# Kernel tuning notes

Hardware: AMD Instinct MI355X
Metric: run time of the kernel (lower is better)

## Reference

```python
import jax, jax.numpy as jnp
import numpy as np

NUM_CLASSES = 81
NMS_THRESHOLD = 0.4
MAX_BOXES = 300
NEG = -1e9  # score used to mark suppressed / background boxes


def setup_inputs() -> dict:
    key = jax.random.key(0)
    k1, k2, k3, k4, k5 = jax.random.split(key, 5)
    N = 300000
    # realistic boxes: centers in [0,800), sizes in [1,101)
    cx = jax.random.uniform(k1, (N,), jnp.float32) * 800.0
    cy = jax.random.uniform(k2, (N,), jnp.float32) * 800.0
    w = jax.random.uniform(k3, (N,), jnp.float32) * 100.0 + 1.0
    h = jax.random.uniform(k4, (N,), jnp.float32) * 100.0 + 1.0
    boxes = jnp.stack([cx - w / 2, cy - h / 2, cx + w / 2, cy + h / 2], axis=-1)
    boxes = boxes[None]  # [1, N, 4]
    classification = jax.random.normal(k5, (1, N, NUM_CLASSES), jnp.float32)
    return {"boxes": boxes, "classification": classification}


def _nms_select(boxes, scores, max_boxes, iou_threshold):
    # boxes: [N,4] (x1,y1,x2,y2); scores: [N]. Greedy NMS, fixed max_boxes iterations.
    x1, y1, x2, y2 = boxes[:, 0], boxes[:, 1], boxes[:, 2], boxes[:, 3]
    areas = jnp.maximum(x2 - x1, 0.0) * jnp.maximum(y2 - y1, 0.0)

    def body(scores_c, _):
        idx = jnp.argmax(scores_c)
        valid = scores_c[idx] > NEG / 2
        b = boxes[idx]
        xx1 = jnp.maximum(b[0], x1)
        yy1 = jnp.maximum(b[1], y1)
        xx2 = jnp.minimum(b[2], x2)
        yy2 = jnp.minimum(b[3], y2)
        inter = jnp.maximum(xx2 - xx1, 0.0) * jnp.maximum(yy2 - yy1, 0.0)
        union = areas[idx] + areas - inter
        iou = inter / jnp.maximum(union, 1e-8)
        # suppress everything overlapping the selected box (includes itself, iou=1)
        new_scores = jnp.where(iou > iou_threshold, NEG, scores_c)
        return new_scores, (idx, valid)

    _, (idxs, valids) = jax.lax.scan(body, scores, None, length=max_boxes)
    return idxs, valids


def reference(boxes, classification):
    b = boxes.reshape(-1, 4)                      # [N,4]
    cls = classification.reshape(-1, NUM_CLASSES)  # [N,C]
    scores = jnp.max(cls, axis=1)                  # [N]
    labels = jnp.argmax(cls, axis=1)               # [N]
    # filter background (label==0) by masking scores instead of dynamic gather
    scores = jnp.where(labels > 0, scores, NEG)
    idxs, valid = _nms_select(b, scores, MAX_BOXES, NMS_THRESHOLD)
    v = valid[:, None].astype(b.dtype)
    out_boxes = b[idxs] * v                        # [max_boxes,4], zero-padded
    out_cls = cls[idxs] * v                        # [max_boxes,C], zero-padded
    return out_boxes[None], out_cls[None]
```

## Files before the change

kernel.cpp:

```cpp
#include <hip/hip_runtime.h>
#include <stdint.h>

#define NUM_CLASSES 81
#define MAX_BOXES 300
#define NEG_SCORE (-1000000000.0f)
#define IOU_THR 0.4f
#define MMAX 2048
#define MWORDS (MMAX / 64)

static constexpr size_t OFF_SCORES = 0;
static constexpr size_t OFF_CAREA  = 0x1F0000;
static constexpr size_t OFF_COARSE = 0x200000;
static constexpr size_t OFF_FINE   = 0x201000;
static constexpr size_t OFF_CTRL   = 0x202000;
static constexpr size_t OFF_RANK   = 0x203000;
static constexpr size_t OFF_KEYS   = 0x208000;
static constexpr size_t OFF_CIDX   = 0x210000;
static constexpr size_t OFF_CBOX   = 0x214000;
static constexpr size_t OFF_ACC    = 0x224000;
static constexpr size_t OFF_MATRIX = 0x228000;

__device__ __forceinline__ uint32_t float_ordered(float f) {
    uint32_t b = __float_as_uint(f);
    return (b & 0x80000000u) ? ~b : (b | 0x80000000u);
}

__device__ __forceinline__ uint64_t readlane_u64(uint64_t v, int srclane) {
    uint32_t lo = (uint32_t)__builtin_amdgcn_readlane((int)(uint32_t)v, srclane);
    uint32_t hi = (uint32_t)__builtin_amdgcn_readlane((int)(uint32_t)(v >> 32), srclane);
    return ((uint64_t)hi << 32) | lo;
}

__global__ void score_kernel(const float* __restrict__ cls, float* __restrict__ scores,
                             uint32_t* __restrict__ coarse, uint32_t* __restrict__ fine,
                             uint32_t* __restrict__ ctrl, uint32_t* __restrict__ rank, int n) {
    if (blockIdx.x == 0) {
        int t = threadIdx.x;
        if (t < 256) { coarse[t] = 0; fine[t] = 0; }
        if (t < 8) ctrl[t] = 0;
        for (int r = t; r < MMAX; r += 256) rank[r] = 0;
    }
    const int q = threadIdx.x & 15;
    const int box = blockIdx.x * 16 + (threadIdx.x >> 4);
    const int cbox = box < n ? box : n - 1;
    const float* row = cls + (size_t)cbox * NUM_CLASSES;

    float v[5];
    #pragma unroll
    for (int it = 0; it < 5; ++it) v[it] = row[it * 16 + q];
    float e80 = row[80];

    float m = v[0];
    #pragma unroll
    for (int it = 1; it < 5; ++it) m = fmaxf(m, v[it]);
    m = (q == 15) ? fmaxf(m, e80) : m;
    m = fmaxf(m, __shfl_xor(m, 1));
    m = fmaxf(m, __shfl_xor(m, 2));
    m = fmaxf(m, __shfl_xor(m, 4));
    m = fmaxf(m, __shfl_xor(m, 8));

    if (q == 0 && box < n) {
        scores[box] = (v[0] == m) ? NEG_SCORE : m;
    }
}

__global__ void coarse_hist_kernel(const float* __restrict__ scores, uint32_t* __restrict__ coarse, int n) {
    __shared__ uint32_t h[256];
    for (int t = threadIdx.x; t < 256; t += blockDim.x) h[t] = 0;
    __syncthreads();
    for (int i = blockIdx.x * blockDim.x + threadIdx.x; i < n; i += gridDim.x * blockDim.x) {
        uint32_t o = float_ordered(scores[i]);
        atomicAdd(&h[o >> 24], 1u);
    }
    __syncthreads();
    for (int t = threadIdx.x; t < 256; t += blockDim.x)
        if (h[t]) atomicAdd(&coarse[t], h[t]);
}

__device__ __forceinline__ int select_coarse(const uint32_t* coarse, uint32_t* above_out) {
    uint32_t s = 0;
    for (int c = 255; c >= 0; --c) {
        uint32_t sc = s + coarse[c];
        if (sc > MMAX) { *above_out = s; return c; }
        s = sc;
    }
    *above_out = s;
    return -1;
}

__global__ void fine_hist_kernel(const float* __restrict__ scores, const uint32_t* __restrict__ coarse,
                                 uint32_t* __restrict__ fine, int n) {
    __shared__ int sC;
    __shared__ uint32_t h[256];
    if (threadIdx.x == 0) {
        uint32_t above;
        sC = select_coarse(coarse, &above);
    }
    for (int t = threadIdx.x; t < 256; t += blockDim.x) h[t] = 0;
    __syncthreads();
    int C = sC;
    if (C < 0) return;
    for (int i = blockIdx.x * blockDim.x + threadIdx.x; i < n; i += gridDim.x * blockDim.x) {
        uint32_t o = float_ordered(scores[i]);
        if ((int)(o >> 24) == C) atomicAdd(&h[(o >> 16) & 255u], 1u);
    }
    __syncthreads();
    for (int t = threadIdx.x; t < 256; t += blockDim.x)
        if (h[t]) atomicAdd(&fine[t], h[t]);
}

__global__ void compact_kernel(const float* __restrict__ scores, const uint32_t* __restrict__ coarse,
                               const uint32_t* __restrict__ fine, uint32_t* __restrict__ ctrl,
                               uint64_t* __restrict__ keys, int n) {
    __shared__ uint32_t sThr;
    if (threadIdx.x == 0) {
        uint32_t above;
        int C = select_coarse(coarse, &above);
        uint32_t thr;
        if (C < 0) {
            thr = 0;
        } else {
            uint32_t R = MMAX - above;
            uint32_t g = 0, F = 0;
            for (int f = 255; f >= 0; --f) {
                uint32_t gf = g + fine[f];
                if (gf > R) { F = (uint32_t)f + 1u; break; }
                g = gf;
            }
            thr = ((uint32_t)C << 8) | F;
        }
        sThr = thr;
    }
    __syncthreads();
    uint32_t thr = sThr;
    for (int i = blockIdx.x * blockDim.x + threadIdx.x; i < n; i += gridDim.x * blockDim.x) {
        uint32_t o = float_ordered(scores[i]);
        if ((o >> 16) >= thr) {
            uint32_t pos = atomicAdd(&ctrl[0], 1u);
            if (pos < MMAX)
                keys[pos] = ((uint64_t)o << 32) | (uint32_t)(~(uint32_t)i);
        }
    }
}

__global__ void rank_partial_kernel(const uint64_t* __restrict__ keys, const uint32_t* __restrict__ ctrl,
                                    uint32_t* __restrict__ rank) {
    __shared__ uint64_t kk[256];
    int M = (int)ctrl[0]; if (M > MMAX) M = MMAX;
    int cbase = blockIdx.x * 256;
    int jbase = blockIdx.y * 256;
    if (cbase >= M || jbase >= M) return;
    int t = threadIdx.x;
    int j = jbase + t;
    kk[t] = (j < M) ? keys[j] : 0ull;
    __syncthreads();
    int c = cbase + t;
    if (c >= M) return;
    uint64_t k = keys[c];
    int cnt = 0;
    #pragma unroll 8
    for (int u = 0; u < 256; ++u) cnt += (kk[u] > k) ? 1 : 0;
    if (cnt) atomicAdd(&rank[c], (uint32_t)cnt);
}

__global__ void scatter_kernel(const uint64_t* __restrict__ keys, const uint32_t* __restrict__ rank,
                               const uint32_t* __restrict__ ctrl, const float* __restrict__ boxes,
                               int* __restrict__ csorted_idx, float4* __restrict__ csorted_box,
                               float* __restrict__ careas) {
    int M = (int)ctrl[0]; if (M > MMAX) M = MMAX;
    int c = blockIdx.x * blockDim.x + threadIdx.x;
    if (c >= M) return;
    uint64_t k = keys[c];
    uint32_t r = rank[c];
    uint32_t idx = ~(uint32_t)k;
    float4 b = *(const float4*)(boxes + (size_t)idx * 4);
    csorted_idx[r] = (int)idx;
    csorted_box[r] = b;
    careas[r] = fmaxf(b.z - b.x, 0.f) * fmaxf(b.w - b.y, 0.f);
}

__global__ void matrix_kernel(const float4* __restrict__ cbox, const float* __restrict__ careas,
                              const uint32_t* __restrict__ ctrl, uint64_t* __restrict__ matrix) {
    int i = blockIdx.x;
    int M = (int)ctrl[0]; if (M > MMAX) M = MMAX;
    if (i >= M) return;
    int lane = threadIdx.x & 63;
    int wave = threadIdx.x >> 6;
    float4 bi = cbox[i];
    float ai = careas[i];
    int w0 = i >> 6;
    for (int w = w0 + wave; w < MWORDS; w += 4) {
        int j = (w << 6) | lane;
        bool sup = false;
        if (j < M) {
            float4 bj = cbox[j];
            float xx1 = fmaxf(bi.x, bj.x);
            float yy1 = fmaxf(bi.y, bj.y);
            float xx2 = fminf(bi.z, bj.z);
            float yy2 = fminf(bi.w, bj.w);
            float inter = fmaxf(xx2 - xx1, 0.f) * fmaxf(yy2 - yy1, 0.f);
            float uni = ai + careas[j] - inter;
            float iou = inter / fmaxf(uni, 1e-8f);
            sup = iou > IOU_THR;
        }
        uint64_t word = __ballot(sup ? 1 : 0);
        if (lane == 0) matrix[(size_t)i * MWORDS + w] = word;
    }
}

typedef const uint32_t __attribute__((address_space(1)))* glb_u32p;
typedef uint32_t __attribute__((address_space(3)))* lds_u32p;

__global__ void __launch_bounds__(64) scan_kernel(
    const uint64_t* __restrict__ matrix, uint32_t* __restrict__ ctrl,
    int* __restrict__ accepted) {
    __shared__ uint64_t sbuf[2][64][MWORDS];
    const int lane = threadIdx.x;
    const int l31 = lane & 31;
    int M = (int)ctrl[0]; if (M > MMAX) M = MMAX;
    uint64_t removed = 0;
    uint64_t wrd = 0;
    int acc = 0;

#define STAGE(BI, BASE)                                                            \
    {                                                                              \
        _Pragma("unroll")                                                          \
        for (int r_ = 0; r_ < 64; ++r_) {                                          \
            const uint32_t* gsrc =                                                 \
                (const uint32_t*)(matrix + (size_t)((BASE) + r_) * MWORDS) + lane; \
            __builtin_amdgcn_global_load_lds((glb_u32p)gsrc,                       \
                                             (lds_u32p)&sbuf[BI][r_][0], 4, 0, 0); \
        }                                                                          \
    }

#define PROCESS(BI, BASE)                                                          \
    {                                                                              \
        uint64_t W[16];                                                            \
        _Pragma("unroll")                                                          \
        for (int w_ = 0; w_ < 16; ++w_) W[w_] = sbuf[BI][w_][l31];                 \
        _Pragma("unroll")                                                          \
        for (int r_ = 0; r_ < 64; ++r_) {                                          \
            int i_ = (BASE) + r_;                                                  \
            uint64_t row = W[r_ & 15];                                             \
            if (r_ + 16 < 64) W[r_ & 15] = sbuf[BI][r_ + 16][l31];                 \
            if (r_ == 0) wrd = readlane_u64(removed, i_ >> 6);                     \
            if (i_ < M && acc < MAX_BOXES && !((wrd >> (i_ & 63)) & 1ull)) {       \
                if (lane == 0) accepted[acc] = i_;                                 \
                removed |= row;                                                    \
                wrd = readlane_u64(removed, i_ >> 6);                              \
                ++acc;                                                             \
            }                                                                      \
        }                                                                          \
    }

    int nblocks = (M + 63) >> 6;
    if (nblocks > 0) {
        STAGE(0, 0);
        asm volatile("s_waitcnt vmcnt(0)" ::: "memory");
        int bi = 0;
        for (int b = 0; b < nblocks && acc < MAX_BOXES; ++b) {
            if (b + 1 < nblocks) STAGE(bi ^ 1, (b + 1) << 6);
            PROCESS(bi, b << 6);
            asm volatile("s_waitcnt vmcnt(0)" ::: "memory");
            bi ^= 1;
        }
    }
#undef STAGE
#undef PROCESS
    if (lane == 0) ctrl[1] = (uint32_t)acc;
}

__global__ void output_kernel(const float* __restrict__ boxes, const float* __restrict__ cls,
                              const int* __restrict__ csorted_idx, const int* __restrict__ accepted,
                              const uint32_t* __restrict__ ctrl, float* __restrict__ out, int total) {
    int e = blockIdx.x * blockDim.x + threadIdx.x;
    if (e >= total) return;
    int acc = (int)ctrl[1];
    float val = 0.0f;
    if (e < MAX_BOXES * 4) {
        int s = e >> 2, f = e & 3;
        if (s < acc) {
            int orig = csorted_idx[accepted[s]];
            val = boxes[(size_t)orig * 4 + f];
        }
    } else {
        int e2 = e - MAX_BOXES * 4;
        int s = e2 / NUM_CLASSES;
        int c = e2 - s * NUM_CLASSES;
        if (s < acc) {
            int orig = csorted_idx[accepted[s]];
            val = cls[(size_t)orig * NUM_CLASSES + c];
        }
    }
    out[e] = val;
}

extern "C" void kernel_launch(void* const* d_in, const int* in_sizes, int n_in,
                              void* d_out, int out_size, void* d_ws, size_t ws_size,
                              hipStream_t stream) {
    const float* boxes = (const float*)d_in[0];
    const float* cls   = (const float*)d_in[1];
    float* out = (float*)d_out;
    const int N = in_sizes[0] / 4;

    char* ws = (char*)d_ws;
    float*     scores      = (float*)(ws + OFF_SCORES);
    float*     careas      = (float*)(ws + OFF_CAREA);
    uint32_t*  coarse      = (uint32_t*)(ws + OFF_COARSE);
    uint32_t*  fine        = (uint32_t*)(ws + OFF_FINE);
    uint32_t*  ctrl        = (uint32_t*)(ws + OFF_CTRL);
    uint32_t*  rank        = (uint32_t*)(ws + OFF_RANK);
    uint64_t*  keys        = (uint64_t*)(ws + OFF_KEYS);
    int*       csorted_idx = (int*)(ws + OFF_CIDX);
    float4*    csorted_box = (float4*)(ws + OFF_CBOX);
    int*       accepted    = (int*)(ws + OFF_ACC);
    uint64_t*  matrix      = (uint64_t*)(ws + OFF_MATRIX);

    score_kernel<<<(N + 15) / 16, 256, 0, stream>>>(cls, scores, coarse, fine, ctrl, rank, N);
    coarse_hist_kernel<<<256, 256, 0, stream>>>(scores, coarse, N);
    fine_hist_kernel<<<256, 256, 0, stream>>>(scores, coarse, fine, N);
    compact_kernel<<<512, 256, 0, stream>>>(scores, coarse, fine, ctrl, keys, N);
    rank_partial_kernel<<<dim3(MMAX / 256, MMAX / 256), 256, 0, stream>>>(keys, ctrl, rank);
    scatter_kernel<<<MMAX / 256, 256, 0, stream>>>(keys, rank, ctrl, boxes, csorted_idx,
                                                   csorted_box, careas);
    matrix_kernel<<<MMAX, 256, 0, stream>>>(csorted_box, careas, ctrl, matrix);
    scan_kernel<<<1, 64, 0, stream>>>(matrix, ctrl, accepted);
    output_kernel<<<(out_size + 255) / 256, 256, 0, stream>>>(boxes, cls, csorted_idx, accepted,
                                                              ctrl, out, out_size);
}
```

Measured before the change: 108.6 us.

## Fuse IoU matrix, greedy scan and output gather into one last-block kernel

Merges the suppression-matrix, sequential scan and output kernels into a single launch. Each block computes its matrix row, then an agent-scope atomic counter elects the last finished block, which runs the greedy scan with accepted indices kept in LDS and writes the output itself. This removes two kernel launches and the global round-trip for accepted indices. In exchange the output gather runs in one block instead of a full grid, and correctness depends on the counter in ctrl[4] being reset each call.

Result: slower. 220.1 us (+102.7%).

```diff
diff --git a/kernel.cpp b/kernel.cpp
--- a/kernel.cpp
+++ b/kernel.cpp
@@ -17,7 +17,6 @@
 static constexpr size_t OFF_KEYS   = 0x208000;
 static constexpr size_t OFF_CIDX   = 0x210000;
 static constexpr size_t OFF_CBOX   = 0x214000;
-static constexpr size_t OFF_ACC    = 0x224000;
 static constexpr size_t OFF_MATRIX = 0x228000;
 
 __device__ __forceinline__ uint32_t float_ordered(float f) {
@@ -179,48 +178,62 @@
     careas[r] = fmaxf(b.z - b.x, 0.f) * fmaxf(b.w - b.y, 0.f);
 }
 
-__global__ void matrix_kernel(const float4* __restrict__ cbox, const float* __restrict__ careas,
-                              const uint32_t* __restrict__ ctrl, uint64_t* __restrict__ matrix) {
-    int i = blockIdx.x;
-    int M = (int)ctrl[0]; if (M > MMAX) M = MMAX;
-    if (i >= M) return;
-    int lane = threadIdx.x & 63;
-    int wave = threadIdx.x >> 6;
-    float4 bi = cbox[i];
-    float ai = careas[i];
-    int w0 = i >> 6;
-    for (int w = w0 + wave; w < MWORDS; w += 4) {
-        int j = (w << 6) | lane;
-        bool sup = false;
-        if (j < M) {
-            float4 bj = cbox[j];
-            float xx1 = fmaxf(bi.x, bj.x);
-            float yy1 = fmaxf(bi.y, bj.y);
-            float xx2 = fminf(bi.z, bj.z);
-            float yy2 = fminf(bi.w, bj.w);
-            float inter = fmaxf(xx2 - xx1, 0.f) * fmaxf(yy2 - yy1, 0.f);
-            float uni = ai + careas[j] - inter;
-            float iou = inter / fmaxf(uni, 1e-8f);
-            sup = iou > IOU_THR;
-        }
-        uint64_t word = __ballot(sup ? 1 : 0);
-        if (lane == 0) matrix[(size_t)i * MWORDS + w] = word;
-    }
-}
-
 typedef const uint32_t __attribute__((address_space(1)))* glb_u32p;
 typedef uint32_t __attribute__((address_space(3)))* lds_u32p;
 
-__global__ void __launch_bounds__(64) scan_kernel(
-    const uint64_t* __restrict__ matrix, uint32_t* __restrict__ ctrl,
-    int* __restrict__ accepted) {
+__global__ void __launch_bounds__(256, 1) tail_kernel(
+    const float4* __restrict__ cbox, const float* __restrict__ careas,
+    uint32_t* __restrict__ ctrl, uint64_t* __restrict__ matrix,
+    const float* __restrict__ boxes, const float* __restrict__ cls,
+    const int* __restrict__ csorted_idx, float* __restrict__ out, int out_total) {
     __shared__ uint64_t sbuf[2][64][MWORDS];
-    const int lane = threadIdx.x;
-    const int l31 = lane & 31;
+    __shared__ int s_accepted[MAX_BOXES];
+    __shared__ int s_acc;
+    __shared__ int s_winner;
+
     int M = (int)ctrl[0]; if (M > MMAX) M = MMAX;
-    uint64_t removed = 0;
-    uint64_t wrd = 0;
-    int acc = 0;
+    const int i = blockIdx.x;
+    const int lane = threadIdx.x & 63;
+    const int wave = threadIdx.x >> 6;
+
+    if (i < M) {
+        float4 bi = cbox[i];
+        float ai = careas[i];
+        int w0 = i >> 6;
+        for (int w = w0 + wave; w < MWORDS; w += 4) {
+            int j = (w << 6) | lane;
+            bool sup = false;
+            if (j < M) {
+                float4 bj = cbox[j];
+                float xx1 = fmaxf(bi.x, bj.x);
+                float yy1 = fmaxf(bi.y, bj.y);
+                float xx2 = fminf(bi.z, bj.z);
+                float yy2 = fminf(bi.w, bj.w);
+                float inter = fmaxf(xx2 - xx1, 0.f) * fmaxf(yy2 - yy1, 0.f);
+                float uni = ai + careas[j] - inter;
+                float iou = inter / fmaxf(uni, 1e-8f);
+                sup = iou > IOU_THR;
+            }
+            uint64_t word = __ballot(sup ? 1 : 0);
+            if (lane == 0) matrix[(size_t)i * MWORDS + w] = word;
+        }
+    }
+
+    __syncthreads();
+    if (threadIdx.x == 0) {
+        __threadfence();
+        uint32_t old = __hip_atomic_fetch_add(&ctrl[4], 1u, __ATOMIC_ACQ_REL,
+                                              __HIP_MEMORY_SCOPE_AGENT);
+        s_winner = (old == (uint32_t)(gridDim.x - 1)) ? 1 : 0;
+    }
+    __syncthreads();
+    if (!s_winner) return;
+
+    if (threadIdx.x < 64) {
+        const int l31 = lane & 31;
+        uint64_t removed = 0;
+        uint64_t wrd = 0;
+        int acc = 0;
 
 #define STAGE(BI, BASE)                                                            \
     {                                                                              \
@@ -245,7 +258,7 @@
             if (r_ + 16 < 64) W[r_ & 15] = sbuf[BI][r_ + 16][l31];                 \
             if (r_ == 0) wrd = readlane_u64(removed, i_ >> 6);                     \
             if (i_ < M && acc < MAX_BOXES && !((wrd >> (i_ & 63)) & 1ull)) {       \
-                if (lane == 0) accepted[acc] = i_;                                 \
+                if (lane == 0) s_accepted[acc] = i_;                               \
                 removed |= row;                                                    \
                 wrd = readlane_u64(removed, i_ >> 6);                              \
                 ++acc;                                                             \
@@ -253,46 +266,46 @@
         }                                                                          \
     }
 
-    int nblocks = (M + 63) >> 6;
-    if (nblocks > 0) {
-        STAGE(0, 0);
-        asm volatile("s_waitcnt vmcnt(0)" ::: "memory");
-        int bi = 0;
-        for (int b = 0; b < nblocks && acc < MAX_BOXES; ++b) {
-            if (b + 1 < nblocks) STAGE(bi ^ 1, (b + 1) << 6);
-            PROCESS(bi, b << 6);
+        int nblocks = (M + 63) >> 6;
+        if (nblocks > 0) {
+            STAGE(0, 0);
             asm volatile("s_waitcnt vmcnt(0)" ::: "memory");
-            bi ^= 1;
-        }
-    }
+            int bi = 0;
+            for (int b = 0; b < nblocks && acc < MAX_BOXES; ++b) {
+                if (b + 1 < nblocks) STAGE(bi ^ 1, (b + 1) << 6);
+                PROCESS(bi, b << 6);
+                asm volatile("s_waitcnt vmcnt(0)" ::: "memory");
+                bi ^= 1;
+            }
+        }
 #undef STAGE
 #undef PROCESS
-    if (lane == 0) ctrl[1] = (uint32_t)acc;
-}
-
-__global__ void output_kernel(const float* __restrict__ boxes, const float* __restrict__ cls,
-                              const int* __restrict__ csorted_idx, const int* __restrict__ accepted,
-                              const uint32_t* __restrict__ ctrl, float* __restrict__ out, int total) {
-    int e = blockIdx.x * blockDim.x + threadIdx.x;
-    if (e >= total) return;
-    int acc = (int)ctrl[1];
-    float val = 0.0f;
-    if (e < MAX_BOXES * 4) {
-        int s = e >> 2, f = e & 3;
-        if (s < acc) {
-            int orig = csorted_idx[accepted[s]];
-            val = boxes[(size_t)orig * 4 + f];
-        }
-    } else {
-        int e2 = e - MAX_BOXES * 4;
-        int s = e2 / NUM_CLASSES;
-        int c = e2 - s * NUM_CLASSES;
-        if (s < acc) {
-            int orig = csorted_idx[accepted[s]];
-            val = cls[(size_t)orig * NUM_CLASSES + c];
-        }
-    }
-    out[e] = val;
+        if (lane == 0) { s_acc = acc; ctrl[1] = (uint32_t)acc; }
+    }
+    __syncthreads();
+
+    {
+        int acc = s_acc;
+        for (int e = threadIdx.x; e < out_total; e += 256) {
+            float val = 0.0f;
+            if (e < MAX_BOXES * 4) {
+                int s = e >> 2, f = e & 3;
+                if (s < acc) {
+                    int orig = csorted_idx[s_accepted[s]];
+                    val = boxes[(size_t)orig * 4 + f];
+                }
+            } else {
+                int e2 = e - MAX_BOXES * 4;
+                int s = e2 / NUM_CLASSES;
+                int c = e2 - s * NUM_CLASSES;
+                if (s < acc) {
+                    int orig = csorted_idx[s_accepted[s]];
+                    val = cls[(size_t)orig * NUM_CLASSES + c];
+                }
+            }
+            out[e] = val;
+        }
+    }
 }
 
 extern "C" void kernel_launch(void* const* d_in, const int* in_sizes, int n_in,
@@ -313,7 +326,6 @@
     uint64_t*  keys        = (uint64_t*)(ws + OFF_KEYS);
     int*       csorted_idx = (int*)(ws + OFF_CIDX);
     float4*    csorted_box = (float4*)(ws + OFF_CBOX);
-    int*       accepted    = (int*)(ws + OFF_ACC);
     uint64_t*  matrix      = (uint64_t*)(ws + OFF_MATRIX);
 
     score_kernel<<<(N + 15) / 16, 256, 0, stream>>>(cls, scores, coarse, fine, ctrl, rank, N);
@@ -323,8 +335,6 @@
     rank_partial_kernel<<<dim3(MMAX / 256, MMAX / 256), 256, 0, stream>>>(keys, ctrl, rank);
     scatter_kernel<<<MMAX / 256, 256, 0, stream>>>(keys, rank, ctrl, boxes, csorted_idx,
                                                    csorted_box, careas);
-    matrix_kernel<<<MMAX, 256, 0, stream>>>(csorted_box, careas, ctrl, matrix);
-    scan_kernel<<<1, 64, 0, stream>>>(matrix, ctrl, accepted);
-    output_kernel<<<(out_size + 255) / 256, 256, 0, stream>>>(boxes, cls, csorted_idx, accepted,
-                                                              ctrl, out, out_size);
-}
+    tail_kernel<<<MMAX, 256, 0, stream>>>(csorted_box, careas, ctrl, matrix,
+                                          boxes, cls, csorted_idx, out, out_size);
+}
```
